# Performance work log

Hardware: AMD Instinct MI355X
Metric: run time of the kernel (lower is better)

## Reference

```python
import jax, jax.numpy as jnp
import numpy as np

SIGMA = 45.0
N, M, D = 4096, 4096, 1024


def setup_inputs() -> dict:
    key = jax.random.key(0)
    k1, k2 = jax.random.split(key)
    inputs = jax.random.normal(k1, (N, D), dtype=jnp.float32)
    samples = jax.random.normal(k2, (M, D), dtype=jnp.float32)
    return {"inputs": inputs, "samples": samples}


def _sq_dists(x, y):
    # ||x_i||^2 + ||y_j||^2 - 2 x_i.y_j  -> [N, M]
    prod = x @ y.T
    xs = jnp.sum(x * x, axis=1)[:, None]
    ys = jnp.sum(y * y, axis=1)[None, :]
    return xs + ys - 2.0 * prod


def reference(inputs, samples):
    n = inputs.shape[0]
    m = samples.shape[0]
    x = inputs.reshape(n, -1)
    y = samples.reshape(m, -1)
    inv_s2 = 1.0 / (SIGMA ** 2)

    k_xx = _sq_dists(x, x)
    k_yy = _sq_dists(y, y)
    k_xy = _sq_dists(x, y)

    # unbiased MMD: exclude diagonal terms of k_xx, k_yy
    exx = jnp.exp(-k_xx * inv_s2)
    eyy = jnp.exp(-k_yy * inv_s2)
    exy = jnp.exp(-k_xy * inv_s2)

    mmd = (jnp.sum(exx) - jnp.sum(jnp.exp(-jnp.diag(k_xx) * inv_s2))) / (n * (n - 1))
    mmd = mmd + (jnp.sum(eyy) - jnp.sum(jnp.exp(-jnp.diag(k_yy) * inv_s2))) / (m * (m - 1))
    mmd = mmd - 2.0 / (n * m) * jnp.sum(exy)
    return mmd
```

## Files before the change

### kernel.cpp

```cpp
#include <hip/hip_runtime.h>
#include <math.h>


typedef _Float16 f16_t;
typedef _Float16 f16x4 __attribute__((ext_vector_type(4)));
typedef _Float16 f16x8 __attribute__((ext_vector_type(8)));
typedef float floatx4 __attribute__((ext_vector_type(4)));

#define NROWS 4096
#define MROWS 4096
#define DDIM  1024
#define BM    128
#define BK    32
#define TILE  (BM * BK)
#define NKT   (DDIM / BK)
#define PSTRIDE (4096 * BK)
#define NT    (NROWS / BM)
#define TRI   (NT * (NT + 1) / 2)
#define NBLK  (2 * TRI + NT * NT)

__global__ __launch_bounds__(256) void convert_kernel(
    const float* __restrict__ X, const float* __restrict__ Y,
    f16_t* __restrict__ Xp, f16_t* __restrict__ Yp,
    float* __restrict__ nx, float* __restrict__ ny,
    double* __restrict__ gsum, int* __restrict__ gcnt) {
    if (blockIdx.x == 0 && threadIdx.x == 0) { *gsum = 0.0; *gcnt = 0; }
    const int wid  = threadIdx.x >> 6;
    const int lane = threadIdx.x & 63;
    const int row  = blockIdx.x * 4 + wid;
    const float* src;
    f16_t* dstp;
    float* nrm;
    int r;
    if (row < NROWS) {
        r = row;         src = X + (size_t)r * DDIM;
        dstp = Xp;  nrm = nx;
    } else {
        r = row - NROWS; src = Y + (size_t)r * DDIM;
        dstp = Yp;  nrm = ny;
    }
    const float4* s4 = (const float4*)src;
    float s = 0.f;
    #pragma unroll
    for (int c = 0; c < 4; c++) {
        float4 v = s4[c * 64 + lane];
        f16x4 h;
        h[0] = (f16_t)v.x; h[1] = (f16_t)v.y;
        h[2] = (f16_t)v.z; h[3] = (f16_t)v.w;
        *(f16x4*)(dstp + (size_t)(c * 8 + (lane >> 3)) * PSTRIDE
                       + (size_t)r * BK + (lane & 7) * 4) = h;
        float h0 = (float)h[0], h1 = (float)h[1];
        float h2 = (float)h[2], h3 = (float)h[3];
        s += h0 * h0 + h1 * h1 + h2 * h2 + h3 * h3;
    }
    #pragma unroll
    for (int off = 32; off > 0; off >>= 1) s += __shfl_down(s, off);
    if (lane == 0) nrm[r] = s;
}

__global__ __launch_bounds__(256) void mmd_mfma(
    const f16_t* __restrict__ Xp, const f16_t* __restrict__ Yp,
    const float* __restrict__ nx, const float* __restrict__ ny,
    double* __restrict__ gsum, int* __restrict__ gcnt,
    float* __restrict__ out) {
    __shared__ __align__(16) f16_t lds[2 * TILE];
    __shared__ double wred[4];

    const int b = ((blockIdx.x & 7) * (NBLK / 8)) + (blockIdx.x >> 3);

    const f16_t *Ap, *Bp;
    const float *nA, *nB;
    int tr, tc;
    double coef;
    if (b < 2 * TRI) {
        int u = (b < TRI) ? b : b - TRI;
        int r = 0;
        while (u >= NT - r) { u -= NT - r; r++; }
        tr = r; tc = r + u;
        double w = (tr == tc) ? 1.0 : 2.0;
        if (b < TRI) { Ap = Xp; Bp = Xp; nA = nx; nB = nx;
                       coef = w / ((double)NROWS * (double)(NROWS - 1)); }
        else         { Ap = Yp; Bp = Yp; nA = ny; nB = ny;
                       coef = w / ((double)MROWS * (double)(MROWS - 1)); }
    } else {
        int u = b - 2 * TRI;
        tr = u >> 5; tc = u & 31;
        Ap = Xp; Bp = Yp; nA = nx; nB = ny;
        coef = -2.0 / ((double)NROWS * (double)MROWS);
    }

    const int t    = threadIdx.x;
    const int wave = t >> 6;
    const int lane = t & 63;
    const int wm   = wave >> 1;
    const int wn   = wave & 1;

    const int lrow = lane >> 2;
    const int schunk = (lane & 3) ^ ((lrow ^ (lrow >> 2)) & 3);
    const f16_t* gsrc[4];
    int ldsoff[4];
    #pragma unroll
    for (int i = 0; i < 4; i++) {
        int idx = wave * 4 + i;
        int tile = idx >> 3;
        int rg   = idx & 7;
        const f16_t* base = tile ? (Bp + (size_t)tc * BM * BK)
                                 : (Ap + (size_t)tr * BM * BK);
        gsrc[i] = base + (size_t)(rg * 16 + lrow) * BK + schunk * 8;
        ldsoff[i] = tile * TILE + rg * 16 * BK;
    }

    const int m    = lane & 15;
    const int quad = lane >> 4;
    const int ac   = quad ^ ((m ^ (m >> 2)) & 3);

    float na[16], nb[4];
    #pragma unroll
    for (int i = 0; i < 4; i++) {
        #pragma unroll
        for (int r = 0; r < 4; r++)
            na[i * 4 + r] = nA[tr * BM + wm * 64 + i * 16 + quad * 4 + r];
        nb[i] = nB[tc * BM + wn * 64 + i * 16 + m];
    }

    floatx4 acc_r[4][4];
    #pragma unroll
    for (int i = 0; i < 4; i++)
        #pragma unroll
        for (int j = 0; j < 4; j++) acc_r[i][j] = (floatx4){0.f, 0.f, 0.f, 0.f};

    for (int kt = 0; kt < NKT; kt++) {
        const size_t ko = (size_t)kt * PSTRIDE;
        __syncthreads();
        #pragma unroll
        for (int i = 0; i < 4; i++) {
            __builtin_amdgcn_global_load_lds(
                (const __attribute__((address_space(1))) void*)(gsrc[i] + ko),
                (__attribute__((address_space(3))) void*)(lds + ldsoff[i]),
                16, 0, 0);
        }
        __syncthreads();

        f16x8 ah[4], bh[4];
        #pragma unroll
        for (int s = 0; s < 4; s++) {
            int arow = wm * 64 + s * 16 + m;
            int brow = wn * 64 + s * 16 + m;
            ah[s] = *(const f16x8*)&lds[arow * BK + ac * 8];
            bh[s] = *(const f16x8*)&lds[TILE + brow * BK + ac * 8];
        }
        #pragma unroll
        for (int i = 0; i < 4; i++)
            #pragma unroll
            for (int j = 0; j < 4; j++)
                acc_r[i][j] = __builtin_amdgcn_mfma_f32_16x16x32_f16(ah[i], bh[j], acc_r[i][j], 0, 0, 0);
    }

    const float inv_s2 = 1.0f / 2025.0f;
    float lsum = 0.f;
    #pragma unroll
    for (int i = 0; i < 4; i++)
        #pragma unroll
        for (int j = 0; j < 4; j++)
            #pragma unroll
            for (int r = 0; r < 4; r++) {
                float arg = (2.f * acc_r[i][j][r] - na[i * 4 + r] - nb[j]) * inv_s2;
                lsum += __expf(arg);
            }

    double d = (double)lsum;
    #pragma unroll
    for (int off = 32; off > 0; off >>= 1) d += __shfl_down(d, off);
    if (lane == 0) wred[wave] = d;
    __syncthreads();
    if (t == 0) {
        double part = (wred[0] + wred[1] + wred[2] + wred[3]) * coef;
        atomicAdd(gsum, part);
        asm volatile("s_waitcnt vmcnt(0)" ::: "memory");
        int old = atomicAdd(gcnt, 1);
        if (old == NBLK - 1) {
            double s = atomicAdd(gsum, 0.0);
            out[0] = (float)(s - 1.0 / (double)(NROWS - 1)
                               - 1.0 / (double)(MROWS - 1));
        }
    }
}

extern "C" void kernel_launch(void* const* d_in, const int* in_sizes, int n_in,
                              void* d_out, int out_size, void* d_ws, size_t ws_size,
                              hipStream_t stream) {
    const float* X = (const float*)d_in[0];
    const float* Y = (const float*)d_in[1];
    float* out = (float*)d_out;

    char* p = (char*)d_ws;
    double* gsum = (double*)p;
    int* gcnt = (int*)(p + sizeof(double));   p += 256;
    float* nx = (float*)p;                    p += (size_t)NROWS * sizeof(float);
    float* ny = (float*)p;                    p += (size_t)MROWS * sizeof(float);
    f16_t* Xp = (f16_t*)p;                    p += (size_t)NROWS * DDIM * sizeof(f16_t);
    f16_t* Yp = (f16_t*)p;

    convert_kernel<<<(NROWS + MROWS) / 4, 256, 0, stream>>>(X, Y, Xp, Yp, nx, ny, gsum, gcnt);
    mmd_mfma<<<NBLK, 256, 0, stream>>>(Xp, Yp, nx, ny, gsum, gcnt, out);
}
```

Measured before the change: 180.1 us.

## Replace atomic last-block reduction with partials buffer and final reduce kernel

Each GEMM block now writes its scaled partial sum to a per-block buffer instead of doing double-precision atomics and a counter-based last-block finish. A separate single-block kernel then tree-reduces those partials. The change also drops the XCD-interleaving block index remap, splits shared memory into separate A and B tiles, and changes the LDS XOR swizzle pattern. The aim is to remove atomic serialization at kernel tail and remove the need to zero the counters in the convert kernel. The cost is an extra kernel launch and possibly worse L2 locality without the block remap.

New measurement: 155.6 us (median of 3 runs). 13.6% less time.

```diff
diff --git a/kernel.cpp b/kernel.cpp
--- a/kernel.cpp
+++ b/kernel.cpp
@@ -22,9 +22,7 @@
 __global__ __launch_bounds__(256) void convert_kernel(
     const float* __restrict__ X, const float* __restrict__ Y,
     f16_t* __restrict__ Xp, f16_t* __restrict__ Yp,
-    float* __restrict__ nx, float* __restrict__ ny,
-    double* __restrict__ gsum, int* __restrict__ gcnt) {
-    if (blockIdx.x == 0 && threadIdx.x == 0) { *gsum = 0.0; *gcnt = 0; }
+    float* __restrict__ nx, float* __restrict__ ny) {
     const int wid  = threadIdx.x >> 6;
     const int lane = threadIdx.x & 63;
     const int row  = blockIdx.x * 4 + wid;
@@ -61,13 +59,12 @@
 __global__ __launch_bounds__(256) void mmd_mfma(
     const f16_t* __restrict__ Xp, const f16_t* __restrict__ Yp,
     const float* __restrict__ nx, const float* __restrict__ ny,
-    double* __restrict__ gsum, int* __restrict__ gcnt,
-    float* __restrict__ out) {
-    __shared__ __align__(16) f16_t lds[2 * TILE];
+    double* __restrict__ partials) {
+    __shared__ __align__(16) f16_t ldsA[TILE];
+    __shared__ __align__(16) f16_t ldsB[TILE];
     __shared__ double wred[4];
 
-    const int b = ((blockIdx.x & 7) * (NBLK / 8)) + (blockIdx.x >> 3);
-
+    const int b = blockIdx.x;
     const f16_t *Ap, *Bp;
     const float *nA, *nB;
     int tr, tc;
@@ -95,10 +92,10 @@
     const int wm   = wave >> 1;
     const int wn   = wave & 1;
 
-    const int lrow = lane >> 2;
-    const int schunk = (lane & 3) ^ ((lrow ^ (lrow >> 2)) & 3);
+    const int lr = lane >> 2;
+    const int lc = (lane & 3) ^ ((lane >> 3) & 3);
     const f16_t* gsrc[4];
-    int ldsoff[4];
+    f16_t* ldst[4];
     #pragma unroll
     for (int i = 0; i < 4; i++) {
         int idx = wave * 4 + i;
@@ -106,13 +103,13 @@
         int rg   = idx & 7;
         const f16_t* base = tile ? (Bp + (size_t)tc * BM * BK)
                                  : (Ap + (size_t)tr * BM * BK);
-        gsrc[i] = base + (size_t)(rg * 16 + lrow) * BK + schunk * 8;
-        ldsoff[i] = tile * TILE + rg * 16 * BK;
+        gsrc[i] = base + (size_t)(rg * 16 + lr) * BK + lc * 8;
+        ldst[i] = (tile ? ldsB : ldsA) + rg * 16 * BK;
     }
 
     const int m    = lane & 15;
     const int quad = lane >> 4;
-    const int ac   = quad ^ ((m ^ (m >> 2)) & 3);
+    const int sw8  = (quad ^ ((m >> 1) & 3)) * 8;
 
     float na[16], nb[4];
     #pragma unroll
@@ -136,7 +133,7 @@
         for (int i = 0; i < 4; i++) {
             __builtin_amdgcn_global_load_lds(
                 (const __attribute__((address_space(1))) void*)(gsrc[i] + ko),
-                (__attribute__((address_space(3))) void*)(lds + ldsoff[i]),
+                (__attribute__((address_space(3))) void*)ldst[i],
                 16, 0, 0);
         }
         __syncthreads();
@@ -144,10 +141,8 @@
         f16x8 ah[4], bh[4];
         #pragma unroll
         for (int s = 0; s < 4; s++) {
-            int arow = wm * 64 + s * 16 + m;
-            int brow = wn * 64 + s * 16 + m;
-            ah[s] = *(const f16x8*)&lds[arow * BK + ac * 8];
-            bh[s] = *(const f16x8*)&lds[TILE + brow * BK + ac * 8];
+            ah[s] = *(const f16x8*)&ldsA[(wm * 64 + s * 16 + m) * BK + sw8];
+            bh[s] = *(const f16x8*)&ldsB[(wn * 64 + s * 16 + m) * BK + sw8];
         }
         #pragma unroll
         for (int i = 0; i < 4; i++)
@@ -173,16 +168,25 @@
     for (int off = 32; off > 0; off >>= 1) d += __shfl_down(d, off);
     if (lane == 0) wred[wave] = d;
     __syncthreads();
+    if (t == 0)
+        partials[b] = (wred[0] + wred[1] + wred[2] + wred[3]) * coef;
+}
+
+__global__ __launch_bounds__(256) void final_reduce(const double* __restrict__ partials,
+                                                    float* __restrict__ out) {
+    __shared__ double red[256];
+    int t = threadIdx.x;
+    double s = 0.0;
+    for (int i = t; i < NBLK; i += 256) s += partials[i];
+    red[t] = s;
+    __syncthreads();
+    for (int off = 128; off > 0; off >>= 1) {
+        if (t < off) red[t] += red[t + off];
+        __syncthreads();
+    }
     if (t == 0) {
-        double part = (wred[0] + wred[1] + wred[2] + wred[3]) * coef;
-        atomicAdd(gsum, part);
-        asm volatile("s_waitcnt vmcnt(0)" ::: "memory");
-        int old = atomicAdd(gcnt, 1);
-        if (old == NBLK - 1) {
-            double s = atomicAdd(gsum, 0.0);
-            out[0] = (float)(s - 1.0 / (double)(NROWS - 1)
-                               - 1.0 / (double)(MROWS - 1));
-        }
+        double mmd = red[0] - 1.0 / (double)(NROWS - 1) - 1.0 / (double)(MROWS - 1);
+        out[0] = (float)mmd;
     }
 }
 
@@ -194,13 +198,13 @@
     float* out = (float*)d_out;
 
     char* p = (char*)d_ws;
-    double* gsum = (double*)p;
-    int* gcnt = (int*)(p + sizeof(double));   p += 256;
+    double* partials = (double*)p;            p += ((size_t)NBLK * sizeof(double) + 255) & ~255ULL;
     float* nx = (float*)p;                    p += (size_t)NROWS * sizeof(float);
     float* ny = (float*)p;                    p += (size_t)MROWS * sizeof(float);
     f16_t* Xp = (f16_t*)p;                    p += (size_t)NROWS * DDIM * sizeof(f16_t);
     f16_t* Yp = (f16_t*)p;
 
-    convert_kernel<<<(NROWS + MROWS) / 4, 256, 0, stream>>>(X, Y, Xp, Yp, nx, ny, gsum, gcnt);
-    mmd_mfma<<<NBLK, 256, 0, stream>>>(Xp, Yp, nx, ny, gsum, gcnt, out);
-}
+    convert_kernel<<<(NROWS + MROWS) / 4, 256, 0, stream>>>(X, Y, Xp, Yp, nx, ny);
+    mmd_mfma<<<NBLK, 256, 0, stream>>>(Xp, Yp, nx, ny, partials);
+    final_reduce<<<1, 256, 0, stream>>>(partials, out);
+}
```
